# Kernel optimization log

Hardware: AMD Instinct MI355X
Metric: run time of the kernel (lower is better)

The kernel has to match this reference:

```python
import jax, jax.numpy as jnp
import numpy as np

N, D_IN = 16384, 1024
E, K = 16, 2
D_EMB, H_UNITS, D_HID = 128, 1024, 512


def setup_inputs() -> dict:
    key = jax.random.key(0)
    ks = jax.random.split(key, 10)
    s = lambda fan_in: 1.0 / np.sqrt(fan_in)
    return {
        "x": jax.random.normal(ks[0], (N, D_IN), jnp.float32),
        "Wr": jax.random.normal(ks[1], (D_IN, D_EMB), jnp.float32) * s(D_IN),
        "br": jnp.zeros((D_EMB,), jnp.float32),
        "expert_embeddings": jax.random.normal(ks[2], (E, D_EMB), jnp.float32) * s(D_EMB),
        "W1": jax.random.normal(ks[3], (E, D_IN, H_UNITS), jnp.float32) * s(D_IN),
        "b1": jnp.zeros((E, H_UNITS), jnp.float32),
        "W2": jax.random.normal(ks[4], (E, H_UNITS, H_UNITS // 2), jnp.float32) * s(H_UNITS),
        "b2": jnp.zeros((E, H_UNITS // 2), jnp.float32),
        "W3": jax.random.normal(ks[5], (E, H_UNITS // 2, D_HID), jnp.float32) * s(H_UNITS // 2),
        "b3": jnp.zeros((E, D_HID), jnp.float32),
    }


def reference(x, Wr, br, expert_embeddings, W1, b1, W2, b2, W3, b3):
    # Router: query per token [N, D_EMB]
    q = x @ Wr + br
    # Negative squared L2 distance to each expert embedding -> scores [N, E]
    d2 = jnp.sum(jnp.square(q[:, None, :] - expert_embeddings[None, :, :]), axis=-1)
    scores = -d2
    # Top-k gating (softmax over the k selected scores only)
    top_k_scores, top_k_idx = jax.lax.top_k(scores, K)        # [N, K]
    gates = jax.nn.softmax(top_k_scores, axis=-1)             # [N, K]
    # Dense all-expert MLP (as the original: every expert on every token)
    h1 = jax.nn.relu(jnp.einsum('nd,edh->enh', x, W1) + b1[:, None, :])   # [E,N,1024]
    h2 = jax.nn.relu(jnp.einsum('enh,ehm->enm', h1, W2) + b2[:, None, :]) # [E,N,512]
    eo = jnp.einsum('enm,emo->eno', h2, W3) + b3[:, None, :]              # [E,N,D_HID]
    eo_t = jnp.transpose(eo, (1, 0, 2))                                   # [N,E,D_HID]
    # Gather top-k expert outputs per token and combine with gates
    sel = jnp.take_along_axis(eo_t, top_k_idx[:, :, None], axis=1)        # [N,K,D_HID]
    combined = jnp.sum(sel * gates[:, :, None], axis=1)                   # [N,D_HID]
    return combined
```

## Files before the change

kernel.cpp:

```cpp
#include <hip/hip_runtime.h>

typedef unsigned short u16;
typedef __attribute__((ext_vector_type(8))) short short8;
typedef __attribute__((ext_vector_type(8))) unsigned short ush8;
typedef __attribute__((ext_vector_type(4))) float f32x4;

#define N_TOK 16384
#define DIN   1024
#define NE    16
#define DEMB  128
#define H1N   1024
#define H2N   512
#define DOUT  512
#define CAP   34816
#define MT    (CAP/128)
#define RBLK  1024

#define OFF_P      0ul
#define OFF_C      65536ul
#define OFF_CTRL   65792ul
#define OFF_E01    66048ul
#define OFF_G01    197120ul
#define OFF_GTOK   328192ul
#define OFF_GGATE  467456ul
#define OFF_TSLOT  606720ul
#define OFF_BH     737792ul
#define OFF_BB     803328ul
#define OFF_W1T    868864ul
#define OFF_W2T    34423296ul
#define OFF_W3T    51200512ul
#define OFF_XBF    59589120ul
#define OFF_H1     93143552ul
#define OFF_H2     164446720ul
#define OFF_EO     OFF_H1

__device__ __forceinline__ u16 f2bf(float f) {
  union { float f; unsigned u; } v; v.f = f;
  unsigned r = v.u + 0x7fff + ((v.u >> 16) & 1);
  return (u16)(r >> 16);
}

__device__ __forceinline__ float bf2f(u16 b) {
  union { unsigned u; float f; } v; v.u = ((unsigned)b) << 16;
  return v.f;
}

__device__ __forceinline__ void async_copy16(const u16* g, u16* l) {
  __builtin_amdgcn_global_load_lds((const __attribute__((address_space(1))) unsigned*)g,
                                   (__attribute__((address_space(3))) unsigned*)l,
                                   16, 0, 0);
}

__global__ void router_prep(const float* __restrict__ Wr, const float* __restrict__ br,
                            const float* __restrict__ emb, float* __restrict__ P,
                            float* __restrict__ c) {
  int idx = blockIdx.x * 256 + threadIdx.x;
  int row = idx >> 4, e = idx & 15;
  float s = 0.f;
  for (int j = 0; j < DEMB; ++j) s += Wr[row * DEMB + j] * emb[e * DEMB + j];
  P[row * NE + e] = 2.f * s;
  if (idx < NE) {
    float cc = 0.f, n2 = 0.f;
    for (int j = 0; j < DEMB; ++j) {
      float ev = emb[idx * DEMB + j];
      cc += br[j] * ev;
      n2 += ev * ev;
    }
    c[idx] = 2.f * cc - n2;
  }
}

__global__ void __launch_bounds__(256) router_score(
    const float* __restrict__ x, const float* __restrict__ P,
    const float* __restrict__ c, int* __restrict__ e01,
    float* __restrict__ g01, int* __restrict__ bhist,
    u16* __restrict__ xbf) {
  __shared__ float xs[16384];
  __shared__ int lh[16];
  int wave = threadIdx.x >> 6, lane = threadIdx.x & 63;
  int e2 = lane & 7, kgl = lane >> 3;
  int tbase = blockIdx.x * 16 + wave * 4;
  float* xw = xs + wave * 4096;

  if (threadIdx.x < 16) lh[threadIdx.x] = 0;

  u16* xbrow = xbf + (size_t)tbase * DIN;
  #pragma unroll
  for (int t = 0; t < 4; ++t) {
    const float* src = x + (size_t)(tbase + t) * DIN;
    #pragma unroll
    for (int q = 0; q < 4; ++q) {
      int g = q * 256 + lane * 4;
      float4 v = *(const float4*)(src + g);
      *(float4*)(xw + t * 1024 + g) = v;
      ushort4 o;
      o.x = f2bf(v.x); o.y = f2bf(v.y); o.z = f2bf(v.z); o.w = f2bf(v.w);
      *(ushort4*)(xbrow + t * DIN + g) = o;
    }
  }
  __syncthreads();

  int te0 = 2 * e2, te1 = te0 + 1;
  float ce0 = c[te0], ce1 = c[te1];
  const float* Pb = P + te0;

  float acc0[4] = {0.f, 0.f, 0.f, 0.f};
  float acc1[4] = {0.f, 0.f, 0.f, 0.f};
  int cbase = kgl * 128;
  #pragma unroll 4
  for (int i = 0; i < 32; ++i) {
    int w = (kgl * 4 + i * 4) & 127;
    int idx = cbase + w;
    float2 pv0 = *(const float2*)(Pb + (size_t)(idx + 0) * NE);
    float2 pv1 = *(const float2*)(Pb + (size_t)(idx + 1) * NE);
    float2 pv2 = *(const float2*)(Pb + (size_t)(idx + 2) * NE);
    float2 pv3 = *(const float2*)(Pb + (size_t)(idx + 3) * NE);
    #pragma unroll
    for (int t = 0; t < 4; ++t) {
      float4 xv = *(const float4*)(xw + t * 1024 + idx);
      acc0[t] = fmaf(xv.x, pv0.x, acc0[t]); acc1[t] = fmaf(xv.x, pv0.y, acc1[t]);
      acc0[t] = fmaf(xv.y, pv1.x, acc0[t]); acc1[t] = fmaf(xv.y, pv1.y, acc1[t]);
      acc0[t] = fmaf(xv.z, pv2.x, acc0[t]); acc1[t] = fmaf(xv.z, pv2.y, acc1[t]);
      acc0[t] = fmaf(xv.w, pv3.x, acc0[t]); acc1[t] = fmaf(xv.w, pv3.y, acc1[t]);
    }
  }

  for (int t = 0; t < 4; ++t) {
    float s0 = acc0[t], s1 = acc1[t];
    #pragma unroll
    for (int off = 8; off <= 32; off <<= 1) {
      s0 += __shfl_xor(s0, off);
      s1 += __shfl_xor(s1, off);
    }
    s0 += ce0; s1 += ce1;
    float hi; int hidx;
    if (s0 >= s1) { hi = s0; hidx = te0; } else { hi = s1; hidx = te1; }
    float m1 = hi; int i1 = hidx;
    #pragma unroll
    for (int off = 1; off < 8; off <<= 1) {
      float so = __shfl_xor(m1, off); int io = __shfl_xor(i1, off);
      if (so > m1 || (so == m1 && io < i1)) { m1 = so; i1 = io; }
    }
    float c2; int c2i;
    if (i1 == te0)      { c2 = s1; c2i = te1; }
    else if (i1 == te1) { c2 = s0; c2i = te0; }
    else                { c2 = hi; c2i = hidx; }
    float m2 = c2; int i2 = c2i;
    #pragma unroll
    for (int off = 1; off < 8; off <<= 1) {
      float so = __shfl_xor(m2, off); int io = __shfl_xor(i2, off);
      if (so > m2 || (so == m2 && io < i2)) { m2 = so; i2 = io; }
    }
    if (lane == 0) {
      int tok = tbase + t;
      float ev = expf(m2 - m1);
      float inv = 1.f / (1.f + ev);
      e01[tok * 2 + 0] = i1; e01[tok * 2 + 1] = i2;
      g01[tok * 2 + 0] = inv; g01[tok * 2 + 1] = ev * inv;
      atomicAdd(&lh[i1], 1);
      atomicAdd(&lh[i2], 1);
    }
  }
  __syncthreads();
  if (threadIdx.x < 16) bhist[blockIdx.x * 16 + threadIdx.x] = lh[threadIdx.x];
}

__global__ void __launch_bounds__(1024) scan_offsets(
    const int* __restrict__ bhist, int* __restrict__ counts,
    int* __restrict__ poff, int* __restrict__ bbase, int* __restrict__ gtok) {
  int t = threadIdx.x;
  int e = t & 15, ch = t >> 4;
  int b0 = ch * 16;
  int s = 0;
  #pragma unroll
  for (int i = 0; i < 16; ++i) s += bhist[(b0 + i) * 16 + e];
  __shared__ int part[64][16];
  __shared__ int chbase[64][16];
  __shared__ int cnt[16];
  __shared__ int pof[16];
  part[ch][e] = s;
  __syncthreads();
  if (t < 16) {
    int run = 0;
    for (int c2 = 0; c2 < 64; ++c2) { chbase[c2][t] = run; run += part[c2][t]; }
    cnt[t] = run;
  }
  __syncthreads();
  if (t == 0) {
    int off = 0;
    for (int e2 = 0; e2 < NE; ++e2) {
      pof[e2] = off;
      poff[e2] = off;
      counts[e2] = cnt[e2];
      off += (cnt[e2] + 127) & ~127;
    }
    poff[NE] = off;
  }
  __syncthreads();
  int padc = ((cnt[e] + 127) & ~127) - cnt[e];
  int pbase = pof[e] + cnt[e];
  if (ch < padc) gtok[pbase + ch] = 0;
  if (ch + 64 < padc) gtok[pbase + ch + 64] = 0;

  int run = pof[e] + chbase[ch][e];
  #pragma unroll
  for (int i = 0; i < 16; ++i) {
    bbase[(b0 + i) * 16 + e] = run;
    run += bhist[(b0 + i) * 16 + e];
  }
}

__global__ void build_lists(const int* __restrict__ e01, const float* __restrict__ g01,
                            const int* __restrict__ bbase, int* __restrict__ gtok,
                            float* __restrict__ ggate, int* __restrict__ tslot) {
  __shared__ int pos[16];
  int tid = threadIdx.x;
  if (tid < 16) pos[tid] = bbase[blockIdx.x * 16 + tid];
  __syncthreads();
  if (tid < 16) {
    int t = blockIdx.x * 16 + tid;
    #pragma unroll
    for (int k = 0; k < 2; ++k) {
      int e = e01[t * 2 + k];
      int p = atomicAdd(&pos[e], 1);
      gtok[p] = t;
      ggate[p] = g01[t * 2 + k];
      tslot[t * 2 + k] = p;
    }
  }
}

template<int K, int N>
__global__ void __launch_bounds__(256) conv_w(const float* __restrict__ W,
                                              u16* __restrict__ WT) {
  __shared__ float tile[64][65];
  int e = blockIdx.z;
  int n0 = blockIdx.x * 64, k0 = blockIdx.y * 64;
  int tid = threadIdx.x;
  const float* Wb = W + (size_t)e * K * N;
  int kr = tid >> 4, nc = (tid & 15) * 4;
  #pragma unroll
  for (int p = 0; p < 4; ++p) {
    int k = p * 16 + kr;
    float4 v = *(const float4*)(Wb + (size_t)(k0 + k) * N + n0 + nc);
    tile[k][nc + 0] = v.x;
    tile[k][nc + 1] = v.y;
    tile[k][nc + 2] = v.z;
    tile[k][nc + 3] = v.w;
  }
  __syncthreads();
  int n = tid >> 2, kc = (tid & 3) * 16;
  ush8 o0, o1;
  #pragma unroll
  for (int j = 0; j < 8; ++j) {
    o0[j] = f2bf(tile[kc + j][n]);
    o1[j] = f2bf(tile[kc + 8 + j][n]);
  }
  u16* dst = WT + (size_t)e * N * K + (size_t)(n0 + n) * K + k0 + kc;
  *(ush8*)dst = o0;
  *(ush8*)(dst + 8) = o1;
}

template<int MODE, bool INDIR>
__global__ void __launch_bounds__(256)
gemm_moe(const u16* __restrict__ A, const u16* __restrict__ Ball,
         const float* __restrict__ bias, u16* __restrict__ Cb,
         const int* __restrict__ poff, const int* __restrict__ counts,
         const int* __restrict__ gtok, int K, int N, int nblk) {
  __shared__ u16 Asm[3][4096];
  __shared__ u16 Bsm[3][4096];

  int bid = blockIdx.x;
  int q = nblk >> 3, r = nblk & 7;
  int xcd = bid & 7, sidx = bid >> 3;
  int wg = (xcd < r ? xcd * (q + 1) : r * (q + 1) + (xcd - r) * q) + sidx;
  int NB = N >> 7;
  int rb = wg / NB, nb = wg - rb * NB;

  int row_base = rb * 128;
  if (row_base >= poff[NE]) return;
  int e = 0;
  while (row_base >= poff[e + 1]) ++e;

  int tid = threadIdx.x;
  int wave = tid >> 6, lane = tid & 63;
  int wm = wave >> 1, wn = wave & 1;
  int fr = lane & 15, kq = lane >> 4;
  int n_base = nb * 128;

  const u16* Brow = Ball + (size_t)e * N * K + (size_t)n_base * K;

  int rr0 = tid >> 2, rr1 = rr0 + 64;
  int ch8 = ((tid & 3) ^ ((rr0 >> 1) & 3)) * 8;
  const u16 *a0, *a1;
  if constexpr (INDIR) {
    a0 = A + (size_t)gtok[row_base + rr0] * K;
    a1 = A + (size_t)gtok[row_base + rr1] * K;
  } else {
    a0 = A + (size_t)(row_base + rr0) * K;
    a1 = A + (size_t)(row_base + rr1) * K;
  }
  const u16* b0 = Brow + (size_t)rr0 * K;
  const u16* b1 = Brow + (size_t)rr1 * K;

  f32x4 acc[4][4];
  #pragma unroll
  for (int m = 0; m < 4; ++m)
    #pragma unroll
    for (int n = 0; n < 4; ++n)
      acc[m][n] = (f32x4){0.f, 0.f, 0.f, 0.f};

  int swz = (fr >> 1) & 3;

  auto stage_tile = [&](int buf, int kt) {
    async_copy16(a0 + kt + ch8, &Asm[buf][tid * 8]);
    async_copy16(a1 + kt + ch8, &Asm[buf][(256 + tid) * 8]);
    async_copy16(b0 + kt + ch8, &Bsm[buf][tid * 8]);
    async_copy16(b1 + kt + ch8, &Bsm[buf][(256 + tid) * 8]);
  };

  stage_tile(0, 0);
  stage_tile(1, 32);

  int nstep = K >> 5;
  int rd = 0, st = 2;
  for (int s = 0; s < nstep; ++s) {
    if (s == nstep - 1)
      asm volatile("s_waitcnt vmcnt(0)\n\ts_barrier" ::: "memory");
    else
      asm volatile("s_waitcnt vmcnt(4)\n\ts_barrier" ::: "memory");
    if (s + 2 < nstep) stage_tile(st, (s + 2) << 5);
    short8 av[4], bv[4];
    #pragma unroll
    for (int m = 0; m < 4; ++m)
      av[m] = *(const short8*)(&Asm[rd][((wm * 64 + m * 16 + fr) * 4 + (kq ^ swz)) * 8]);
    #pragma unroll
    for (int n = 0; n < 4; ++n)
      bv[n] = *(const short8*)(&Bsm[rd][((wn * 64 + n * 16 + fr) * 4 + (kq ^ swz)) * 8]);
    #pragma unroll
    for (int m = 0; m < 4; ++m)
      #pragma unroll
      for (int n = 0; n < 4; ++n)
        acc[m][n] = __builtin_amdgcn_mfma_f32_16x16x32_bf16(av[m], bv[n], acc[m][n], 0, 0, 0);
    rd = rd == 2 ? 0 : rd + 1;
    st = st == 2 ? 0 : st + 1;
  }

  int crow = (lane >> 4) * 4;
  int ccol = lane & 15;
  const float* be = bias + (size_t)e * N;
  #pragma unroll
  for (int m = 0; m < 4; ++m) {
    int gr0 = row_base + wm * 64 + m * 16 + crow;
    #pragma unroll
    for (int n = 0; n < 4; ++n) {
      int gc = n_base + wn * 64 + n * 16 + ccol;
      float bvs = be[gc];
      #pragma unroll
      for (int r2 = 0; r2 < 4; ++r2) {
        float v = acc[m][n][r2] + bvs;
        if constexpr (MODE == 0) v = v > 0.f ? v : 0.f;
        Cb[(size_t)(gr0 + r2) * N + gc] = f2bf(v);
      }
    }
  }
}

__global__ void __launch_bounds__(256) combine_out(
    const u16* __restrict__ eo, const int* __restrict__ tslot,
    const float* __restrict__ g01, float* __restrict__ out) {
  int wave = threadIdx.x >> 6, lane = threadIdx.x & 63;
  int tok = blockIdx.x * 4 + wave;
  int s0 = tslot[tok * 2 + 0], s1 = tslot[tok * 2 + 1];
  float g0 = g01[tok * 2 + 0], g1 = g01[tok * 2 + 1];
  ush8 v0 = *(const ush8*)(eo + (size_t)s0 * DOUT + lane * 8);
  ush8 v1 = *(const ush8*)(eo + (size_t)s1 * DOUT + lane * 8);
  float* o = out + (size_t)tok * DOUT + lane * 8;
  float4 ov0, ov1;
  ov0.x = g0 * bf2f(v0[0]) + g1 * bf2f(v1[0]);
  ov0.y = g0 * bf2f(v0[1]) + g1 * bf2f(v1[1]);
  ov0.z = g0 * bf2f(v0[2]) + g1 * bf2f(v1[2]);
  ov0.w = g0 * bf2f(v0[3]) + g1 * bf2f(v1[3]);
  ov1.x = g0 * bf2f(v0[4]) + g1 * bf2f(v1[4]);
  ov1.y = g0 * bf2f(v0[5]) + g1 * bf2f(v1[5]);
  ov1.z = g0 * bf2f(v0[6]) + g1 * bf2f(v1[6]);
  ov1.w = g0 * bf2f(v0[7]) + g1 * bf2f(v1[7]);
  ((float4*)o)[0] = ov0;
  ((float4*)o)[1] = ov1;
}

extern "C" void kernel_launch(void* const* d_in, const int* in_sizes, int n_in,
                              void* d_out, int out_size, void* d_ws, size_t ws_size,
                              hipStream_t stream) {
  const float* x   = (const float*)d_in[0];
  const float* Wr  = (const float*)d_in[1];
  const float* br  = (const float*)d_in[2];
  const float* emb = (const float*)d_in[3];
  const float* W1  = (const float*)d_in[4];
  const float* b1  = (const float*)d_in[5];
  const float* W2  = (const float*)d_in[6];
  const float* b2  = (const float*)d_in[7];
  const float* W3  = (const float*)d_in[8];
  const float* b3  = (const float*)d_in[9];
  float* out = (float*)d_out;
  char* ws = (char*)d_ws;

  float* P      = (float*)(ws + OFF_P);
  float* c      = (float*)(ws + OFF_C);
  int*   counts = (int*)(ws + OFF_CTRL);
  int*   poff   = (int*)(ws + OFF_CTRL + 128);
  int*   e01    = (int*)(ws + OFF_E01);
  float* g01    = (float*)(ws + OFF_G01);
  int*   gtok   = (int*)(ws + OFF_GTOK);
  float* ggate  = (float*)(ws + OFF_GGATE);
  int*   tslot  = (int*)(ws + OFF_TSLOT);
  int*   bhist  = (int*)(ws + OFF_BH);
  int*   bbase  = (int*)(ws + OFF_BB);
  u16*   W1T    = (u16*)(ws + OFF_W1T);
  u16*   W2T    = (u16*)(ws + OFF_W2T);
  u16*   W3T    = (u16*)(ws + OFF_W3T);
  u16*   xbf    = (u16*)(ws + OFF_XBF);
  u16*   h1     = (u16*)(ws + OFF_H1);
  u16*   h2     = (u16*)(ws + OFF_H2);
  u16*   eo16   = (u16*)(ws + OFF_EO);

  conv_w<DIN, H1N><<<dim3(H1N / 64, DIN / 64, NE), 256, 0, stream>>>(W1, W1T);
  conv_w<H1N, H2N><<<dim3(H2N / 64, H1N / 64, NE), 256, 0, stream>>>(W2, W2T);
  conv_w<H2N, DOUT><<<dim3(DOUT / 64, H2N / 64, NE), 256, 0, stream>>>(W3, W3T);

  router_prep<<<64, 256, 0, stream>>>(Wr, br, emb, P, c);
  router_score<<<RBLK, 256, 0, stream>>>(x, P, c, e01, g01, bhist, xbf);
  scan_offsets<<<1, 1024, 0, stream>>>(bhist, counts, poff, bbase, gtok);
  build_lists<<<RBLK, 64, 0, stream>>>(e01, g01, bbase, gtok, ggate, tslot);

  int nb1 = (H1N / 128) * MT;
  int nb2 = (H2N / 128) * MT;
  int nb3 = (DOUT / 128) * MT;
  gemm_moe<0, true><<<nb1, 256, 0, stream>>>(xbf, W1T, b1, h1,
                                             poff, counts, gtok, DIN, H1N, nb1);
  gemm_moe<0, false><<<nb2, 256, 0, stream>>>(h1, W2T, b2, h2,
                                              poff, counts, nullptr, H1N, H2N, nb2);
  gemm_moe<2, false><<<nb3, 256, 0, stream>>>(h2, W3T, b3, eo16,
                                              poff, counts, nullptr, H2N, DOUT, nb3);
  combine_out<<<N_TOK / 4, 256, 0, stream>>>(eo16, tslot, g01, out);
}
```

Before: 280.2 us.

## Enlarge MoE GEMM row tile to 256 with 512 threads and double buffering

The expert GEMMs now use a 256-row by 128-column tile per block with 8 waves instead of 128x128 with 4 waves. Each block therefore reuses every staged weight tile across twice as many token rows, which is meant to cut weight traffic and halve the number of blocks. Per-expert row padding grows to multiples of 256, and the workspace layout is reorganised so h2 reuses the W1T region. The triple-buffered async pipeline with explicit vmcnt waits is replaced by double buffering with a full barrier every step. This risks less latency hiding and more wasted rows on padding.

```diff
diff --git a/kernel.cpp b/kernel.cpp
--- a/kernel.cpp
+++ b/kernel.cpp
@@ -12,8 +12,8 @@
 #define H1N   1024
 #define H2N   512
 #define DOUT  512
-#define CAP   34816
-#define MT    (CAP/128)
+#define CAP   36864
+#define RB    (CAP/256)
 #define RBLK  1024
 
 #define OFF_P      0ul
@@ -22,17 +22,17 @@
 #define OFF_E01    66048ul
 #define OFF_G01    197120ul
 #define OFF_GTOK   328192ul
-#define OFF_GGATE  467456ul
-#define OFF_TSLOT  606720ul
-#define OFF_BH     737792ul
-#define OFF_BB     803328ul
-#define OFF_W1T    868864ul
-#define OFF_W2T    34423296ul
-#define OFF_W3T    51200512ul
-#define OFF_XBF    59589120ul
-#define OFF_H1     93143552ul
-#define OFF_H2     164446720ul
+#define OFF_GGATE  475648ul
+#define OFF_TSLOT  623104ul
+#define OFF_BH     754176ul
+#define OFF_BB     819712ul
+#define OFF_W2T    885248ul
+#define OFF_W3T    17662464ul
+#define OFF_W1T    26051072ul
+#define OFF_XBF    59605504ul
+#define OFF_H1     93159936ul
 #define OFF_EO     OFF_H1
+#define OFF_H2     OFF_W1T
 
 __device__ __forceinline__ u16 f2bf(float f) {
   union { float f; unsigned u; } v; v.f = f;
@@ -192,15 +192,14 @@
       pof[e2] = off;
       poff[e2] = off;
       counts[e2] = cnt[e2];
-      off += (cnt[e2] + 127) & ~127;
+      off += (cnt[e2] + 255) & ~255;
     }
     poff[NE] = off;
   }
   __syncthreads();
-  int padc = ((cnt[e] + 127) & ~127) - cnt[e];
+  int padc = ((cnt[e] + 255) & ~255) - cnt[e];
   int pbase = pof[e] + cnt[e];
-  if (ch < padc) gtok[pbase + ch] = 0;
-  if (ch + 64 < padc) gtok[pbase + ch + 64] = 0;
+  for (int i = ch; i < padc; i += 64) gtok[pbase + i] = 0;
 
   int run = pof[e] + chbase[ch][e];
   #pragma unroll
@@ -262,13 +261,13 @@
 }
 
 template<int MODE, bool INDIR>
-__global__ void __launch_bounds__(256)
+__global__ void __launch_bounds__(512)
 gemm_moe(const u16* __restrict__ A, const u16* __restrict__ Ball,
          const float* __restrict__ bias, u16* __restrict__ Cb,
          const int* __restrict__ poff, const int* __restrict__ counts,
          const int* __restrict__ gtok, int K, int N, int nblk) {
-  __shared__ u16 Asm[3][4096];
-  __shared__ u16 Bsm[3][4096];
+  __shared__ u16 Asm[2][8192];
+  __shared__ u16 Bsm[2][4096];
 
   int bid = blockIdx.x;
   int q = nblk >> 3, r = nblk & 7;
@@ -277,7 +276,7 @@
   int NB = N >> 7;
   int rb = wg / NB, nb = wg - rb * NB;
 
-  int row_base = rb * 128;
+  int row_base = rb * 256;
   if (row_base >= poff[NE]) return;
   int e = 0;
   while (row_base >= poff[e + 1]) ++e;
@@ -290,18 +289,17 @@
 
   const u16* Brow = Ball + (size_t)e * N * K + (size_t)n_base * K;
 
-  int rr0 = tid >> 2, rr1 = rr0 + 64;
+  int rr0 = tid >> 2;
   int ch8 = ((tid & 3) ^ ((rr0 >> 1) & 3)) * 8;
   const u16 *a0, *a1;
   if constexpr (INDIR) {
     a0 = A + (size_t)gtok[row_base + rr0] * K;
-    a1 = A + (size_t)gtok[row_base + rr1] * K;
+    a1 = A + (size_t)gtok[row_base + rr0 + 128] * K;
   } else {
     a0 = A + (size_t)(row_base + rr0) * K;
-    a1 = A + (size_t)(row_base + rr1) * K;
+    a1 = A + (size_t)(row_base + rr0 + 128) * K;
   }
   const u16* b0 = Brow + (size_t)rr0 * K;
-  const u16* b1 = Brow + (size_t)rr1 * K;
 
   f32x4 acc[4][4];
   #pragma unroll
@@ -314,36 +312,31 @@
 
   auto stage_tile = [&](int buf, int kt) {
     async_copy16(a0 + kt + ch8, &Asm[buf][tid * 8]);
-    async_copy16(a1 + kt + ch8, &Asm[buf][(256 + tid) * 8]);
+    async_copy16(a1 + kt + ch8, &Asm[buf][(512 + tid) * 8]);
     async_copy16(b0 + kt + ch8, &Bsm[buf][tid * 8]);
-    async_copy16(b1 + kt + ch8, &Bsm[buf][(256 + tid) * 8]);
   };
 
   stage_tile(0, 0);
-  stage_tile(1, 32);
+  __syncthreads();
 
   int nstep = K >> 5;
-  int rd = 0, st = 2;
+  int cur = 0;
   for (int s = 0; s < nstep; ++s) {
-    if (s == nstep - 1)
-      asm volatile("s_waitcnt vmcnt(0)\n\ts_barrier" ::: "memory");
-    else
-      asm volatile("s_waitcnt vmcnt(4)\n\ts_barrier" ::: "memory");
-    if (s + 2 < nstep) stage_tile(st, (s + 2) << 5);
+    if (s + 1 < nstep) stage_tile(cur ^ 1, (s + 1) << 5);
     short8 av[4], bv[4];
     #pragma unroll
     for (int m = 0; m < 4; ++m)
-      av[m] = *(const short8*)(&Asm[rd][((wm * 64 + m * 16 + fr) * 4 + (kq ^ swz)) * 8]);
+      av[m] = *(const short8*)(&Asm[cur][((wm * 64 + m * 16 + fr) * 4 + (kq ^ swz)) * 8]);
     #pragma unroll
     for (int n = 0; n < 4; ++n)
-      bv[n] = *(const short8*)(&Bsm[rd][((wn * 64 + n * 16 + fr) * 4 + (kq ^ swz)) * 8]);
+      bv[n] = *(const short8*)(&Bsm[cur][((wn * 64 + n * 16 + fr) * 4 + (kq ^ swz)) * 8]);
     #pragma unroll
     for (int m = 0; m < 4; ++m)
       #pragma unroll
       for (int n = 0; n < 4; ++n)
         acc[m][n] = __builtin_amdgcn_mfma_f32_16x16x32_bf16(av[m], bv[n], acc[m][n], 0, 0, 0);
-    rd = rd == 2 ? 0 : rd + 1;
-    st = st == 2 ? 0 : st + 1;
+    __syncthreads();
+    cur ^= 1;
   }
 
   int crow = (lane >> 4) * 4;
@@ -433,14 +426,14 @@
   scan_offsets<<<1, 1024, 0, stream>>>(bhist, counts, poff, bbase, gtok);
   build_lists<<<RBLK, 64, 0, stream>>>(e01, g01, bbase, gtok, ggate, tslot);
 
-  int nb1 = (H1N / 128) * MT;
-  int nb2 = (H2N / 128) * MT;
-  int nb3 = (DOUT / 128) * MT;
-  gemm_moe<0, true><<<nb1, 256, 0, stream>>>(xbf, W1T, b1, h1,
+  int nb1 = (H1N / 128) * RB;
+  int nb2 = (H2N / 128) * RB;
+  int nb3 = (DOUT / 128) * RB;
+  gemm_moe<0, true><<<nb1, 512, 0, stream>>>(xbf, W1T, b1, h1,
                                              poff, counts, gtok, DIN, H1N, nb1);
-  gemm_moe<0, false><<<nb2, 256, 0, stream>>>(h1, W2T, b2, h2,
+  gemm_moe<0, false><<<nb2, 512, 0, stream>>>(h1, W2T, b2, h2,
                                               poff, counts, nullptr, H1N, H2N, nb2);
-  gemm_moe<2, false><<<nb3, 256, 0, stream>>>(h2, W3T, b3, eo16,
+  gemm_moe<2, false><<<nb3, 512, 0, stream>>>(h2, W3T, b3, eo16,
                                               poff, counts, nullptr, H2N, DOUT, nb3);
   combine_out<<<N_TOK / 4, 256, 0, stream>>>(eo16, tslot, g01, out);
 }
```

Measured after the change: 298.0 us. +6.3%, slower.
